# Kernel tuning notes

Hardware: AMD Instinct MI355X
Metric: run time of the kernel (lower is better)

Reference implementation:

```python
import jax, jax.numpy as jnp
import numpy as np

# ---- hyperparameters matching init_kwargs / input_specs ----
K = 16          # max neighbors kept per node (avg degree)
ALPHA = 0.5     # FGW trade-off (POT default used in the repo)
FW_ITERS = 5    # Frank-Wolfe (conditional-gradient) outer iterations
SK_ITERS = 20   # log-domain Sinkhorn inner iterations
REG = 0.1       # entropic regularization for the inner OT solve
NEG = -1e9      # "log(0)" for masked (padded) neighborhood slots


def build_neighbors(edge_index, n, k):
    """Fixed-size (padded) neighbor table from a COO edge list."""
    src, dst = edge_index[0], edge_index[1]
    order = jnp.argsort(src)
    s_src, s_dst = src[order], dst[order]
    ids = jnp.arange(n)
    start = jnp.searchsorted(s_src, ids)
    end = jnp.searchsorted(s_src, ids, side='right')
    cnt = jnp.minimum(end - start, k)                       # [n]
    pos = start[:, None] + jnp.arange(k)[None, :]           # [n,k]
    valid = jnp.arange(k)[None, :] < cnt[:, None]           # [n,k]
    nbrs = s_dst[jnp.clip(pos, 0, s_src.shape[0] - 1)]      # [n,k]
    return nbrs, valid


def reference(x, edge_index, templates, templates_features):
    n, d = x.shape
    nbrs, valid = build_neighbors(edge_index, n, K)
    # local node set per node: self + up to K neighbors -> K1 = K+1 slots
    S = jnp.concatenate([jnp.arange(n)[:, None], nbrs], axis=1)            # [n,K1]
    mask = jnp.concatenate([jnp.ones((n, 1), bool), valid], axis=1)        # [n,K1]
    mf = mask.astype(x.dtype)

    # local subgraph adjacency: A[i,a,b] = 1 iff edge S[i,a] -> S[i,b]
    nbrs_of = nbrs[S]                                                      # [n,K1,K]
    valid_of = valid[S]
    eq = (nbrs_of[:, :, None, :] == S[:, None, :, None]) & valid_of[:, :, None, :]
    C1 = eq.any(-1).astype(x.dtype) * mf[:, :, None] * mf[:, None, :]      # [n,K1,K1]

    F1 = x[S] * mf[:, :, None]                                             # [n,K1,d]
    F2 = templates_features                                                # [T,t,d]
    # squared-euclidean feature cost M[i,T,a,b] = ||F1[i,a]-F2[T,b]||^2
    M = (jnp.sum(F1 ** 2, -1)[:, None, :, None]
         + jnp.sum(F2 ** 2, -1)[None, :, None, :]
         - 2.0 * jnp.einsum('nad,tbd->ntab', F1, F2))                      # [n,T,K1,t]

    cnt1 = mf.sum(1)                                                       # [n] (>=1: self)
    p = mf / cnt1[:, None]                                                 # [n,K1] uniform masked
    t_n = templates.shape[1]
    q = jnp.full((t_n,), 1.0 / t_n, x.dtype)
    C2 = templates                                                         # [T,t,t]

    # GW square-loss decomposition (POT): tens = constC - 2*C1 @ T @ C2^T
    constC = (jnp.einsum('nab,nb->na', C1 ** 2, p)[:, None, :, None]
              + jnp.einsum('tab,b->ta', C2 ** 2, q)[None, :, None, :])     # [n,T,K1,t]

    def tens_of(T):
        tmp = jnp.einsum('nac,ntcd->ntad', C1, T)
        cross = jnp.einsum('ntad,tbd->ntab', tmp, C2)
        return constC - 2.0 * cross

    logp = jnp.where(mask, -jnp.log(cnt1)[:, None], NEG)[:, None, :]       # [n,1,K1]
    logq = -jnp.log(jnp.asarray(t_n, x.dtype))                             # scalar

    def sinkhorn(G):
        logK = -G / REG                                                    # [n,T,K1,t]
        f = jnp.zeros(G.shape[:3], G.dtype)
        g = jnp.zeros(G.shape[:2] + (t_n,), G.dtype)
        def body(_, fg):
            f, g = fg
            g = logq - jax.nn.logsumexp(logK + f[..., :, None], axis=-2)
            f = logp - jax.nn.logsumexp(logK + g[..., None, :], axis=-1)
            return (f, g)
        f, g = jax.lax.fori_loop(0, SK_ITERS, body, (f, g))
        return jnp.exp(f[..., :, None] + g[..., None, :] + logK)

    T0 = p[:, None, :, None] * q[None, None, None, :]                      # [n,1->T,K1,t]
    T0 = jnp.broadcast_to(T0, M.shape)

    def fw_step(T, k):
        tens = tens_of(T)
        G = (1.0 - ALPHA) * M + 2.0 * ALPHA * tens                         # FGW gradient
        Tn = sinkhorn(G)                                                   # linear-min oracle
        gamma = 2.0 / (k + 2.0)
        return (1.0 - gamma) * T + gamma * Tn, None

    T, _ = jax.lax.scan(fw_step, T0, jnp.arange(FW_ITERS, dtype=x.dtype))

    tens = tens_of(T)
    dist = ((1.0 - ALPHA) * jnp.sum(M * T, axis=(-2, -1))
            + ALPHA * jnp.sum(tens * T, axis=(-2, -1)))                    # [n,T]
    return dist


def setup_inputs() -> dict:
    key = jax.random.key(0)
    k1, k2, k3, k4 = jax.random.split(key, 4)
    n, d, e = 10000, 128, 160000
    n_T, t_n = 10, 10
    x = jax.random.normal(k1, (n, d), jnp.float32)
    edge_index = jax.random.randint(k2, (2, e), 0, n, jnp.int64)
    templates = jax.random.uniform(k3, (n_T, t_n, t_n), jnp.float32)
    templates_features = jax.random.normal(k4, (n_T, t_n, d), jnp.float32)
    return {"x": x, "edge_index": edge_index,
            "templates": templates, "templates_features": templates_features}
```

## Files before the change

### kernel.cpp

```cpp
#include <hip/hip_runtime.h>
#include <math.h>

#define NNODE 10000
#define NEDGE 160000
#define KNB   16
#define K1    17
#define NT    10
#define TN    10
#define DF    128
#define CAP   64
#define NEG_BIG (-1e9f)

#define LOGQ2      (-3.32192809489f)
#define KB_SCALE   (-14.4269504089f)
#define CR_SCALE   (28.8539008178f)
#define G_SCALE    (-0.069314718056f)
#define LN2        0.69314718056f
#define TINYF      1e-30f

#if defined(__has_builtin)
#if __has_builtin(__builtin_amdgcn_exp2f)
#define EXP2F(x) __builtin_amdgcn_exp2f(x)
#endif
#if __has_builtin(__builtin_amdgcn_rcpf)
#define RCPF(x) __builtin_amdgcn_rcpf(x)
#endif
#endif
#ifndef EXP2F
#define EXP2F(x) __expf((x) * LN2)
#endif
#ifndef RCPF
#define RCPF(x) (1.0f / (x))
#endif
#define LOG2F(x) __log2f(x)

#define WSYNC() asm volatile("s_waitcnt lgkmcnt(0)" ::: "memory")

__device__ __forceinline__ float2 pk_add(float2 a, float2 b) { return make_float2(a.x + b.x, a.y + b.y); }
__device__ __forceinline__ float2 pk_sub(float2 a, float2 b) { return make_float2(a.x - b.x, a.y - b.y); }
__device__ __forceinline__ float2 pk_mul(float2 a, float2 b) { return make_float2(a.x * b.x, a.y * b.y); }
__device__ __forceinline__ float2 pk_max(float2 a, float2 b) { return make_float2(fmaxf(a.x, b.x), fmaxf(a.y, b.y)); }
__device__ __forceinline__ float2 pk_fma(float2 a, float2 b, float2 c) { return make_float2(fmaf(a.x, b.x, c.x), fmaf(a.y, b.y, c.y)); }
__device__ __forceinline__ float2 pk_exp2(float2 a) { return make_float2(EXP2F(a.x), EXP2F(a.y)); }
__device__ __forceinline__ float clamp120(float x) { return fminf(120.f, fmaxf(-120.f, x)); }

__device__ __forceinline__ int detect_wide(const int* ei) {
  int z = 0;
#pragma unroll
  for (int i = 0; i < 32; ++i) z |= ei[2 * i + 1];
  return z == 0;
}

__global__ void __launch_bounds__(256) k_prep(const int* __restrict__ ei,
                                              int* cnt, int* ebuf,
                                              const float* __restrict__ x,
                                              const float* __restrict__ tf,
                                              const float* __restrict__ tmpl,
                                              float* __restrict__ dots,
                                              float* __restrict__ nxv,
                                              float* __restrict__ nF2,
                                              float* __restrict__ Bq) {
  __shared__ float xs[64][DF];
  const int tid = threadIdx.x;
  if (blockIdx.x < 625) {
    int e = blockIdx.x * 256 + tid;
    int wide = detect_wide(ei);
    int s = wide ? ei[2 * e] : ei[e];
    int pos = atomicAdd(&cnt[s], 1);
    if (pos < CAP) ebuf[s * CAP + pos] = e;
    return;
  }
  const int db = blockIdx.x - 625;
  if (db == 0 && tid < NT * TN) {
    const float* fp = tf + (size_t)tid * DF;
    float s = 0.f;
    for (int d = 0; d < DF; ++d) { float v = fp[d]; s += v * v; }
    nF2[tid] = s;
    const float* cp = tmpl + (size_t)tid * TN;
    float s2 = 0.f;
    for (int c = 0; c < TN; ++c) { float v = cp[c]; s2 += v * v; }
    Bq[tid] = 0.1f * s2;
  }
  const int nb = db * 64;
  const int nvalid = (NNODE - nb) < 64 ? (NNODE - nb) : 64;
  {
    const float4* xg = (const float4*)(x + (size_t)nb * DF);
    float4* xl = (float4*)&xs[0][0];
    for (int i = tid; i < nvalid * (DF / 4); i += 256) xl[i] = xg[i];
  }
  __syncthreads();
  for (int o = tid; o < nvalid * (NT * TN); o += 256) {
    int n = o / (NT * TN);
    int tb = o - n * (NT * TN);
    const float4* fp = (const float4*)(tf + (size_t)tb * DF);
    const float4* xp = (const float4*)&xs[n][0];
    float s = 0.f;
#pragma unroll
    for (int d = 0; d < DF / 4; ++d) {
      float4 a = xp[d], f = fp[d];
      s += a.x * f.x + a.y * f.y + a.z * f.z + a.w * f.w;
    }
    dots[(size_t)(nb + n) * (NT * TN) + tb] = s;
  }
  if (tid < nvalid) {
    const float4* xp = (const float4*)&xs[tid][0];
    float s = 0.f;
#pragma unroll
    for (int d = 0; d < DF / 4; ++d) {
      float4 a = xp[d];
      s += a.x * a.x + a.y * a.y + a.z * a.z + a.w * a.w;
    }
    nxv[nb + tid] = s;
  }
}

__global__ void k_select(const int* ei, const int* cnt, const int* ebuf,
                         int* nbrs, int* kcnt, int* Sg) {
  int i = blockIdx.x * blockDim.x + threadIdx.x;
  if (i >= NNODE) return;
  int wide = detect_wide(ei);
  int c = cnt[i]; c = c > CAP ? CAP : c;
  int best[KNB];
  int m = 0;
  for (int j = 0; j < c; ++j) {
    int e = ebuf[i * CAP + j];
    if (m < KNB) {
      int p = m++;
      while (p > 0 && best[p - 1] > e) { best[p] = best[p - 1]; --p; }
      best[p] = e;
    } else if (e < best[KNB - 1]) {
      int p = KNB - 1;
      while (p > 0 && best[p - 1] > e) { best[p] = best[p - 1]; --p; }
      best[p] = e;
    }
  }
  kcnt[i] = m;
  Sg[i * K1 + 0] = i;
  for (int j = 0; j < KNB; ++j) {
    int v = 0;
    if (j < m) {
      int e = best[j];
      v = wide ? ei[2 * (NEDGE + e)] : ei[NEDGE + e];
    }
    nbrs[i * KNB + j] = v;
    Sg[i * K1 + 1 + j] = v;
  }
}

__global__ void __launch_bounds__(256) k_c1b(const int* __restrict__ nbrs,
                                             const int* __restrict__ kcnt,
                                             const int* __restrict__ Sg,
                                             unsigned int* __restrict__ bitsG,
                                             float* __restrict__ Ag) {
  int idx = blockIdx.x * 256 + threadIdx.x;
  if (idx >= NNODE * K1) return;
  int i = idx / K1;
  int a = idx - i * K1;
  int kc = kcnt[i];
  unsigned int vmask = (kc >= KNB) ? 0x1FFFFu : ((2u << kc) - 1u);
  unsigned int bits = 0;
  bool va = (a == 0) || (a - 1 < kc);
  if (va) {
    int S[K1];
#pragma unroll
    for (int b = 0; b < K1; ++b) S[b] = Sg[i * K1 + b];
    int u = S[a];
    int ku = kcnt[u];
    const int* np = nbrs + (size_t)u * KNB;
    for (int j = 0; j < ku; ++j) {
      int w = np[j];
#pragma unroll
      for (int b = 0; b < K1; ++b) bits |= (S[b] == w) ? (1u << b) : 0u;
    }
    bits &= vmask;
  }
  bitsG[idx] = bits;
  Ag[idx] = (float)__popc(bits) / (float)(1 + kc);
}

__global__ void __launch_bounds__(128, 3) k_main(
    const float* __restrict__ tmpl,
    const int* __restrict__ kcnt, const int* __restrict__ Sg,
    const unsigned int* __restrict__ bitsG, const float* __restrict__ Ag,
    const float* __restrict__ dots, const float* __restrict__ nxv,
    const float* __restrict__ nF2, const float* __restrict__ Bq,
    float* __restrict__ out)
{
  __shared__ float KT[2 * 5 * 244];
  __shared__ float fL[2][5][20];
  __shared__ float gL[2][5][12];
  __shared__ float accL[2][5][TN];
  __shared__ float uL[2][5][20];
  __shared__ float wL[2][5][12];

  const int wv = threadIdx.x >> 6;
  const int lane = threadIdx.x & 63;
  int p = lane / 10;
  const int b = lane - p * 10;
  const bool act = (p < 5);
  if (!act) p = 4;
  const int node = blockIdx.x;
  const int t = wv * 5 + p;
  const int tb = t * TN + b;
  float* KTp = &KT[(wv * 5 + p) * 244];

  const int kc = kcnt[node];
  const float cnt1 = (float)(1 + kc);
  const float inv_cnt1 = 1.f / cnt1;
  const float logp2v = -LOG2F(cnt1);
  const float lp2_r0 = ((b == 0) || (b - 1 < kc)) ? logp2v : NEG_BIG;
  const float lp2_r1 = ((9 + b) < kc) ? logp2v : NEG_BIG;

  float2 c2v[5];
  {
    const float2* cp = (const float2*)(tmpl + (size_t)tb * TN);
#pragma unroll
    for (int j = 0; j < 5; ++j) c2v[j] = cp[j];
  }
  const float Bb = Bq[tb];
  const float nf2b = nF2[tb];

  float2 Kb2v[8]; float kb16;
  float2 Tpv[8];  float tp16;
  unsigned int bw[K1];
#pragma unroll
  for (int a = 0; a < K1; ++a) {
    bool va = (a == 0) || (a - 1 < kc);
    int sa = Sg[node * K1 + a];
    float Ma = (va ? (nxv[sa] - 2.f * dots[(size_t)sa * (NT * TN) + tb]) : 0.f) + nf2b;
    float base = 0.5f * Ma + Ag[node * K1 + a] + Bb;
    float kv = KB_SCALE * base;
    float tv = va ? (inv_cnt1 * 0.1f) : 0.f;
    if (a == 16) { kb16 = kv; tp16 = tv; }
    else if (a & 1) { Kb2v[a >> 1].y = kv; Tpv[a >> 1].y = tv; }
    else { Kb2v[a >> 1].x = kv; Tpv[a >> 1].x = tv; }
    bw[a] = bitsG[node * K1 + a];
  }

  float2 Kc2v[8]; float k16 = 0.f;
  float2 Kr0v[5], Kr1v[5];
  float2 gr[5];
  float g2 = 0.f, fr0 = 0.f, fr1 = 0.f;

#pragma unroll 1
  for (int k = 0; k < 6; ++k) {
    if (act) {
#pragma unroll
      for (int a = 0; a < 16; ++a) KTp[a * 12 + b] = (a & 1) ? Tpv[a >> 1].y : Tpv[a >> 1].x;
      KTp[16 * 12 + b] = tp16;
    }
    WSYNC();
    float R[K1];
#pragma unroll
    for (int c = 0; c < K1; ++c) {
      const float* row = &KTp[c * 12];
      float4 u0 = *(const float4*)row;
      float4 u1 = *(const float4*)(row + 4);
      float2 u2 = *(const float2*)(row + 8);
      float2 acc = pk_mul(make_float2(u0.x, u0.y), c2v[0]);
      acc = pk_fma(make_float2(u0.z, u0.w), c2v[1], acc);
      acc = pk_fma(make_float2(u1.x, u1.y), c2v[2], acc);
      acc = pk_fma(make_float2(u1.z, u1.w), c2v[3], acc);
      acc = pk_fma(u2, c2v[4], acc);
      R[c] = acc.x + acc.y;
    }
#pragma unroll
    for (int a = 0; a < K1; ++a) {
      float cr = 0.f;
      unsigned int m = bw[a];
      if (m) {
#pragma unroll
        for (int c = 0; c < K1; ++c)
          if (m & (1u << c)) cr += R[c];
      }
      float base = (a == 16) ? kb16 : ((a & 1) ? Kb2v[a >> 1].y : Kb2v[a >> 1].x);
      float val = base + CR_SCALE * cr;
      if (a == 16) k16 = val;
      else if (a & 1) Kc2v[a >> 1].y = val;
      else Kc2v[a >> 1].x = val;
    }

    if (k == 5) {
      float acc = 0.f;
#pragma unroll
      for (int a = 0; a < K1; ++a) {
        bool va = (a == 0) || (a - 1 < kc);
        int sa = Sg[node * K1 + a];
        float Ma = (va ? (nxv[sa] - 2.f * dots[(size_t)sa * (NT * TN) + tb]) : 0.f) + nf2b;
        float kcv = (a == 16) ? k16 : ((a & 1) ? Kc2v[a >> 1].y : Kc2v[a >> 1].x);
        float tpv = (a == 16) ? tp16 : ((a & 1) ? Tpv[a >> 1].y : Tpv[a >> 1].x);
        acc += tpv * (0.25f * Ma + 0.5f * (G_SCALE * kcv));
      }
      if (act) accL[wv][p][b] = acc;
      WSYNC();
      if (lane < 5) {
        float s = 0.f;
#pragma unroll
        for (int j = 0; j < TN; ++j) s += accL[wv][lane][j];
        out[node * NT + wv * 5 + lane] = s;
      }
      return;
    }

    WSYNC();
    if (act) {
#pragma unroll
      for (int a = 0; a < 16; ++a) KTp[a * 12 + b] = (a & 1) ? Kc2v[a >> 1].y : Kc2v[a >> 1].x;
      KTp[16 * 12 + b] = k16;
    }
    WSYNC();
    {
      const float* r0 = &KTp[b * 12];
      float4 u0 = *(const float4*)r0;
      float4 u1 = *(const float4*)(r0 + 4);
      float2 u2 = *(const float2*)(r0 + 8);
      Kr0v[0] = make_float2(u0.x, u0.y); Kr0v[1] = make_float2(u0.z, u0.w);
      Kr0v[2] = make_float2(u1.x, u1.y); Kr0v[3] = make_float2(u1.z, u1.w);
      Kr0v[4] = u2;
      const float* r1 = &KTp[(10 + b) * 12];
      float4 w0 = *(const float4*)r1;
      float4 w1 = *(const float4*)(r1 + 4);
      float2 w2 = *(const float2*)(r1 + 8);
      Kr1v[0] = make_float2(w0.x, w0.y); Kr1v[1] = make_float2(w0.z, w0.w);
      Kr1v[2] = make_float2(w1.x, w1.y); Kr1v[3] = make_float2(w1.z, w1.w);
      Kr1v[4] = w2;
    }

#pragma unroll 1
    for (int it = 0; it < 2; ++it) {
      float2 v[8]; float v16;
      if (it == 0) {
#pragma unroll
        for (int i = 0; i < 8; ++i) v[i] = Kc2v[i];
        v16 = k16;
      } else {
        float4 f0 = *(const float4*)&fL[wv][p][0];
        float4 f1 = *(const float4*)&fL[wv][p][4];
        float4 f2 = *(const float4*)&fL[wv][p][8];
        float4 f3 = *(const float4*)&fL[wv][p][12];
        float fx = fL[wv][p][16];
        v[0] = pk_add(Kc2v[0], make_float2(f0.x, f0.y));
        v[1] = pk_add(Kc2v[1], make_float2(f0.z, f0.w));
        v[2] = pk_add(Kc2v[2], make_float2(f1.x, f1.y));
        v[3] = pk_add(Kc2v[3], make_float2(f1.z, f1.w));
        v[4] = pk_add(Kc2v[4], make_float2(f2.x, f2.y));
        v[5] = pk_add(Kc2v[5], make_float2(f2.z, f2.w));
        v[6] = pk_add(Kc2v[6], make_float2(f3.x, f3.y));
        v[7] = pk_add(Kc2v[7], make_float2(f3.z, f3.w));
        v16 = k16 + fx;
      }
      float2 m01 = pk_max(pk_max(v[0], v[1]), pk_max(v[2], v[3]));
      float2 m23 = pk_max(pk_max(v[4], v[5]), pk_max(v[6], v[7]));
      float2 mm = pk_max(m01, m23);
      float mx = fmaxf(fmaxf(mm.x, mm.y), v16);
      float2 mxb = make_float2(mx, mx);
      float2 ss = pk_exp2(pk_sub(v[0], mxb));
      ss = pk_add(ss, pk_exp2(pk_sub(v[1], mxb)));
      ss = pk_add(ss, pk_exp2(pk_sub(v[2], mxb)));
      ss = pk_add(ss, pk_exp2(pk_sub(v[3], mxb)));
      ss = pk_add(ss, pk_exp2(pk_sub(v[4], mxb)));
      ss = pk_add(ss, pk_exp2(pk_sub(v[5], mxb)));
      ss = pk_add(ss, pk_exp2(pk_sub(v[6], mxb)));
      ss = pk_add(ss, pk_exp2(pk_sub(v[7], mxb)));
      float s = ss.x + ss.y + EXP2F(v16 - mx);
      g2 = LOGQ2 - mx - LOG2F(s);
      if (act) gL[wv][p][b] = g2;
      WSYNC();
      {
        float4 g0 = *(const float4*)&gL[wv][p][0];
        float4 g1 = *(const float4*)&gL[wv][p][4];
        float2 gx = *(const float2*)&gL[wv][p][8];
        gr[0] = make_float2(g0.x, g0.y); gr[1] = make_float2(g0.z, g0.w);
        gr[2] = make_float2(g1.x, g1.y); gr[3] = make_float2(g1.z, g1.w);
        gr[4] = gx;
      }
      float2 w0[5], w1[5];
#pragma unroll
      for (int j = 0; j < 5; ++j) w0[j] = pk_add(Kr0v[j], gr[j]);
#pragma unroll
      for (int j = 0; j < 5; ++j) w1[j] = pk_add(Kr1v[j], gr[j]);
      float2 a01 = pk_max(pk_max(w0[0], w0[1]), pk_max(w0[2], w0[3]));
      a01 = pk_max(a01, w0[4]);
      float mxa = fmaxf(a01.x, a01.y);
      float2 b01 = pk_max(pk_max(w1[0], w1[1]), pk_max(w1[2], w1[3]));
      b01 = pk_max(b01, w1[4]);
      float mxb2 = fmaxf(b01.x, b01.y);
      float2 mab = make_float2(mxa, mxa);
      float2 mbb = make_float2(mxb2, mxb2);
      float2 sx = pk_exp2(pk_sub(w0[0], mab));
      sx = pk_add(sx, pk_exp2(pk_sub(w0[1], mab)));
      sx = pk_add(sx, pk_exp2(pk_sub(w0[2], mab)));
      sx = pk_add(sx, pk_exp2(pk_sub(w0[3], mab)));
      sx = pk_add(sx, pk_exp2(pk_sub(w0[4], mab)));
      float2 sy = pk_exp2(pk_sub(w1[0], mbb));
      sy = pk_add(sy, pk_exp2(pk_sub(w1[1], mbb)));
      sy = pk_add(sy, pk_exp2(pk_sub(w1[2], mbb)));
      sy = pk_add(sy, pk_exp2(pk_sub(w1[3], mbb)));
      sy = pk_add(sy, pk_exp2(pk_sub(w1[4], mbb)));
      fr0 = lp2_r0 - mxa - LOG2F(sx.x + sx.y);
      fr1 = lp2_r1 - mxb2 - LOG2F(sy.x + sy.y);
      if (act) {
        fL[wv][p][b] = fr0;
        if (b < 7) fL[wv][p][10 + b] = fr1;
      }
      WSYNC();
    }

    float2 Kcsv[8]; float kcs16;
    float P00, P01, Q0;
    float2 Krs01[10];
    {
      float4 F0 = *(const float4*)&fL[wv][p][0];
      float4 F1 = *(const float4*)&fL[wv][p][4];
      float4 F2 = *(const float4*)&fL[wv][p][8];
      float4 F3 = *(const float4*)&fL[wv][p][12];
      float f16v = fL[wv][p][16];
      float2 q[8];
      q[0] = pk_add(Kc2v[0], make_float2(F0.x, F0.y));
      q[1] = pk_add(Kc2v[1], make_float2(F0.z, F0.w));
      q[2] = pk_add(Kc2v[2], make_float2(F1.x, F1.y));
      q[3] = pk_add(Kc2v[3], make_float2(F1.z, F1.w));
      q[4] = pk_add(Kc2v[4], make_float2(F2.x, F2.y));
      q[5] = pk_add(Kc2v[5], make_float2(F2.z, F2.w));
      q[6] = pk_add(Kc2v[6], make_float2(F3.x, F3.y));
      q[7] = pk_add(Kc2v[7], make_float2(F3.z, F3.w));
      float q16 = k16 + f16v;
      float2 qm = pk_max(pk_max(pk_max(q[0], q[1]), pk_max(q[2], q[3])),
                         pk_max(pk_max(q[4], q[5]), pk_max(q[6], q[7])));
      float sigma = fmaxf(fmaxf(qm.x, qm.y), q16);
      float2 sgb = make_float2(sigma, sigma);
#pragma unroll
      for (int i = 0; i < 8; ++i) Kcsv[i] = pk_exp2(pk_sub(q[i], sgb));
      kcs16 = EXP2F(q16 - sigma);
      Q0 = EXP2F(clamp120(LOGQ2 - sigma - g2));
      float2 a0[5], a1[5];
#pragma unroll
      for (int j = 0; j < 5; ++j) a0[j] = pk_add(Kr0v[j], gr[j]);
#pragma unroll
      for (int j = 0; j < 5; ++j) a1[j] = pk_add(Kr1v[j], gr[j]);
      float2 r0m = pk_max(pk_max(a0[0], a0[1]), pk_max(a0[2], a0[3]));
      r0m = pk_max(r0m, a0[4]);
      float rho0 = fmaxf(r0m.x, r0m.y);
      float2 r1m = pk_max(pk_max(a1[0], a1[1]), pk_max(a1[2], a1[3]));
      r1m = pk_max(r1m, a1[4]);
      float rho1 = fmaxf(r1m.x, r1m.y);
#pragma unroll
      for (int j = 0; j < 5; ++j) {
        Krs01[2 * j]     = make_float2(EXP2F(a0[j].x - rho0), EXP2F(a1[j].x - rho1));
        Krs01[2 * j + 1] = make_float2(EXP2F(a0[j].y - rho0), EXP2F(a1[j].y - rho1));
      }
      P00 = EXP2F(clamp120((lp2_r0 - rho0) - fr0));
      P01 = EXP2F(clamp120((lp2_r1 - rho1) - fr1));
    }

    float Slast, t0, t1;
    {
      float2 S2 = pk_add(pk_add(pk_add(Kcsv[0], Kcsv[1]), pk_add(Kcsv[2], Kcsv[3])),
                         pk_add(pk_add(Kcsv[4], Kcsv[5]), pk_add(Kcsv[6], Kcsv[7])));
      float S = fmaxf(S2.x + S2.y + kcs16, TINYF);
      Slast = S;
      float wb = Q0 * RCPF(S);
      if (act) wL[wv][p][b] = wb;
      WSYNC();
      float4 W0 = *(const float4*)&wL[wv][p][0];
      float4 W1 = *(const float4*)&wL[wv][p][4];
      float2 W2 = *(const float2*)&wL[wv][p][8];
      float2 t01 = pk_mul(Krs01[0], make_float2(W0.x, W0.x));
      t01 = pk_fma(Krs01[1], make_float2(W0.y, W0.y), t01);
      t01 = pk_fma(Krs01[2], make_float2(W0.z, W0.z), t01);
      t01 = pk_fma(Krs01[3], make_float2(W0.w, W0.w), t01);
      t01 = pk_fma(Krs01[4], make_float2(W1.x, W1.x), t01);
      t01 = pk_fma(Krs01[5], make_float2(W1.y, W1.y), t01);
      t01 = pk_fma(Krs01[6], make_float2(W1.z, W1.z), t01);
      t01 = pk_fma(Krs01[7], make_float2(W1.w, W1.w), t01);
      t01 = pk_fma(Krs01[8], make_float2(W2.x, W2.x), t01);
      t01 = pk_fma(Krs01[9], make_float2(W2.y, W2.y), t01);
      t0 = t01.x; t1 = t01.y;
    }
#pragma unroll 1
    for (int it = 0; it < 17; ++it) {
      float u0 = P00 * RCPF(fmaxf(t0, TINYF));
      float u1 = P01 * RCPF(fmaxf(t1, TINYF));
      if (act) {
        uL[wv][p][b] = u0;
        if (b < 7) uL[wv][p][10 + b] = u1;
      }
      WSYNC();
      float4 U0 = *(const float4*)&uL[wv][p][0];
      float4 U1 = *(const float4*)&uL[wv][p][4];
      float4 U2 = *(const float4*)&uL[wv][p][8];
      float4 U3 = *(const float4*)&uL[wv][p][12];
      float u16f = uL[wv][p][16];
      float2 S2 = pk_mul(Kcsv[0], make_float2(U0.x, U0.y));
      S2 = pk_fma(Kcsv[1], make_float2(U0.z, U0.w), S2);
      S2 = pk_fma(Kcsv[2], make_float2(U1.x, U1.y), S2);
      S2 = pk_fma(Kcsv[3], make_float2(U1.z, U1.w), S2);
      S2 = pk_fma(Kcsv[4], make_float2(U2.x, U2.y), S2);
      S2 = pk_fma(Kcsv[5], make_float2(U2.z, U2.w), S2);
      S2 = pk_fma(Kcsv[6], make_float2(U3.x, U3.y), S2);
      S2 = pk_fma(Kcsv[7], make_float2(U3.z, U3.w), S2);
      float S = fmaxf(S2.x + S2.y + kcs16 * u16f, TINYF);
      Slast = S;
      float wb = Q0 * RCPF(S);
      if (act) wL[wv][p][b] = wb;
      WSYNC();
      float4 W0 = *(const float4*)&wL[wv][p][0];
      float4 W1 = *(const float4*)&wL[wv][p][4];
      float2 W2 = *(const float2*)&wL[wv][p][8];
      float2 t01 = pk_mul(Krs01[0], make_float2(W0.x, W0.x));
      t01 = pk_fma(Krs01[1], make_float2(W0.y, W0.y), t01);
      t01 = pk_fma(Krs01[2], make_float2(W0.z, W0.z), t01);
      t01 = pk_fma(Krs01[3], make_float2(W0.w, W0.w), t01);
      t01 = pk_fma(Krs01[4], make_float2(W1.x, W1.x), t01);
      t01 = pk_fma(Krs01[5], make_float2(W1.y, W1.y), t01);
      t01 = pk_fma(Krs01[6], make_float2(W1.z, W1.z), t01);
      t01 = pk_fma(Krs01[7], make_float2(W1.w, W1.w), t01);
      t01 = pk_fma(Krs01[8], make_float2(W2.x, W2.x), t01);
      t01 = pk_fma(Krs01[9], make_float2(W2.y, W2.y), t01);
      t0 = t01.x; t1 = t01.y;
    }

    {
      float u0 = P00 * RCPF(fmaxf(t0, TINYF));
      float u1 = P01 * RCPF(fmaxf(t1, TINYF));
      if (act) {
        uL[wv][p][b] = u0;
        if (b < 7) uL[wv][p][10 + b] = u1;
      }
      WSYNC();
      float4 U0 = *(const float4*)&uL[wv][p][0];
      float4 U1 = *(const float4*)&uL[wv][p][4];
      float4 U2 = *(const float4*)&uL[wv][p][8];
      float4 U3 = *(const float4*)&uL[wv][p][12];
      float u16f = uL[wv][p][16];
      const float sb = 0.1f * RCPF(Slast);
      const float gam = 2.f / ((float)k + 2.f);
      const float om = 1.f - gam;
      const float gs = gam * sb;
      const float2 omb = make_float2(om, om);
      const float2 gsb = make_float2(gs, gs);
      float2 uu[8];
      uu[0] = make_float2(U0.x, U0.y); uu[1] = make_float2(U0.z, U0.w);
      uu[2] = make_float2(U1.x, U1.y); uu[3] = make_float2(U1.z, U1.w);
      uu[4] = make_float2(U2.x, U2.y); uu[5] = make_float2(U2.z, U2.w);
      uu[6] = make_float2(U3.x, U3.y); uu[7] = make_float2(U3.z, U3.w);
#pragma unroll
      for (int i = 0; i < 8; ++i)
        Tpv[i] = pk_fma(omb, Tpv[i], pk_mul(gsb, pk_mul(Kcsv[i], uu[i])));
      tp16 = om * tp16 + gs * kcs16 * u16f;
    }
  }
}

extern "C" void kernel_launch(void* const* d_in, const int* in_sizes, int n_in,
                              void* d_out, int out_size, void* d_ws, size_t ws_size,
                              hipStream_t stream) {
  const float* x    = (const float*)d_in[0];
  const int*   ei   = (const int*)d_in[1];
  const float* tmpl = (const float*)d_in[2];
  const float* tf   = (const float*)d_in[3];
  float* out = (float*)d_out;

  int* cnt  = (int*)d_ws;
  int* ebuf = cnt + NNODE;
  int* nbrs = ebuf + (size_t)NNODE * CAP;
  int* kcnt = nbrs + (size_t)NNODE * KNB;
  int* Sg   = kcnt + NNODE;
  unsigned int* bits = (unsigned int*)(Sg + (size_t)NNODE * K1);
  float* Ag   = (float*)(bits + (size_t)NNODE * K1);
  float* dots = Ag + (size_t)NNODE * K1;
  float* nxv  = dots + (size_t)NNODE * (NT * TN);
  float* nF2  = nxv + NNODE;
  float* Bq   = nF2 + NT * TN;

  hipMemsetAsync(cnt, 0, NNODE * sizeof(int), stream);
  k_prep<<<625 + (NNODE + 63) / 64, 256, 0, stream>>>(ei, cnt, ebuf, x, tf, tmpl,
                                                      dots, nxv, nF2, Bq);
  k_select<<<(NNODE + 255) / 256, 256, 0, stream>>>(ei, cnt, ebuf, nbrs, kcnt, Sg);
  k_c1b<<<(NNODE * K1 + 255) / 256, 256, 0, stream>>>(nbrs, kcnt, Sg, bits, Ag);
  k_main<<<NNODE, 128, 0, stream>>>(tmpl, kcnt, Sg, bits, Ag, dots, nxv, nF2, Bq, out);
}
```

Before: 605.6 us.

## Pack two nodes per 256-thread block and interleave u/T vectors as pairs

k_main now handles two nodes per block with 256 threads, and launch bounds change to (256,5) to raise occupancy. Per-wave LDS strides shrink from 244 to 204 floats. The transport plan and scaled-kernel registers are repacked into a 10-entry float2 layout pairing row j with row j+10. This lets u values be written as one float2 store and read as five float4 loads instead of scalar stores with a tail element. The tighter register budget implied by the new launch bound risks spills in a register-heavy kernel.

```diff
diff --git a/kernel.cpp b/kernel.cpp
--- a/kernel.cpp
+++ b/kernel.cpp
@@ -178,7 +178,7 @@
   Ag[idx] = (float)__popc(bits) / (float)(1 + kc);
 }
 
-__global__ void __launch_bounds__(128, 3) k_main(
+__global__ void __launch_bounds__(256, 5) k_main(
     const float* __restrict__ tmpl,
     const int* __restrict__ kcnt, const int* __restrict__ Sg,
     const unsigned int* __restrict__ bitsG, const float* __restrict__ Ag,
@@ -186,12 +186,12 @@
     const float* __restrict__ nF2, const float* __restrict__ Bq,
     float* __restrict__ out)
 {
-  __shared__ float KT[2 * 5 * 244];
-  __shared__ float fL[2][5][20];
-  __shared__ float gL[2][5][12];
-  __shared__ float accL[2][5][TN];
-  __shared__ float uL[2][5][20];
-  __shared__ float wL[2][5][12];
+  __shared__ float KT[4 * 5 * 204 + 48];
+  __shared__ float fL[4][5][20];
+  __shared__ float gL[4][5][12];
+  __shared__ float uL[4][5][20];
+  __shared__ float wL[4][5][12];
+  __shared__ float accL[4][5][TN];
 
   const int wv = threadIdx.x >> 6;
   const int lane = threadIdx.x & 63;
@@ -199,10 +199,11 @@
   const int b = lane - p * 10;
   const bool act = (p < 5);
   if (!act) p = 4;
-  const int node = blockIdx.x;
-  const int t = wv * 5 + p;
+  const int node = blockIdx.x * 2 + (wv >> 1);
+  const int h = wv & 1;
+  const int t = h * 5 + p;
   const int tb = t * TN + b;
-  float* KTp = &KT[(wv * 5 + p) * 244];
+  float* KTp = &KT[(wv * 5 + p) * 204];
 
   const int kc = kcnt[node];
   const float cnt1 = (float)(1 + kc);
@@ -221,7 +222,9 @@
   const float nf2b = nF2[tb];
 
   float2 Kb2v[8]; float kb16;
-  float2 Tpv[8];  float tp16;
+  float2 Tp2[10];
+#pragma unroll
+  for (int j = 0; j < 10; ++j) Tp2[j] = make_float2(0.f, 0.f);
   unsigned int bw[K1];
 #pragma unroll
   for (int a = 0; a < K1; ++a) {
@@ -231,9 +234,10 @@
     float base = 0.5f * Ma + Ag[node * K1 + a] + Bb;
     float kv = KB_SCALE * base;
     float tv = va ? (inv_cnt1 * 0.1f) : 0.f;
-    if (a == 16) { kb16 = kv; tp16 = tv; }
-    else if (a & 1) { Kb2v[a >> 1].y = kv; Tpv[a >> 1].y = tv; }
-    else { Kb2v[a >> 1].x = kv; Tpv[a >> 1].x = tv; }
+    if (a == 16) kb16 = kv;
+    else if (a & 1) Kb2v[a >> 1].y = kv;
+    else Kb2v[a >> 1].x = kv;
+    if (a < 10) Tp2[a].x = tv; else Tp2[a - 10].y = tv;
     bw[a] = bitsG[node * K1 + a];
   }
 
@@ -246,8 +250,8 @@
   for (int k = 0; k < 6; ++k) {
     if (act) {
 #pragma unroll
-      for (int a = 0; a < 16; ++a) KTp[a * 12 + b] = (a & 1) ? Tpv[a >> 1].y : Tpv[a >> 1].x;
-      KTp[16 * 12 + b] = tp16;
+      for (int a = 0; a < K1; ++a)
+        KTp[a * 12 + b] = (a < 10) ? Tp2[a].x : Tp2[a - 10].y;
     }
     WSYNC();
     float R[K1];
@@ -288,7 +292,7 @@
         int sa = Sg[node * K1 + a];
         float Ma = (va ? (nxv[sa] - 2.f * dots[(size_t)sa * (NT * TN) + tb]) : 0.f) + nf2b;
         float kcv = (a == 16) ? k16 : ((a & 1) ? Kc2v[a >> 1].y : Kc2v[a >> 1].x);
-        float tpv = (a == 16) ? tp16 : ((a & 1) ? Tpv[a >> 1].y : Tpv[a >> 1].x);
+        float tpv = (a < 10) ? Tp2[a].x : Tp2[a - 10].y;
         acc += tpv * (0.25f * Ma + 0.5f * (G_SCALE * kcv));
       }
       if (act) accL[wv][p][b] = acc;
@@ -297,7 +301,7 @@
         float s = 0.f;
 #pragma unroll
         for (int j = 0; j < TN; ++j) s += accL[wv][lane][j];
-        out[node * NT + wv * 5 + lane] = s;
+        out[node * NT + h * 5 + lane] = s;
       }
       return;
     }
@@ -406,7 +410,7 @@
       WSYNC();
     }
 
-    float2 Kcsv[8]; float kcs16;
+    float2 Kcs2[10];
     float P00, P01, Q0;
     float2 Krs01[10];
     {
@@ -415,23 +419,27 @@
       float4 F2 = *(const float4*)&fL[wv][p][8];
       float4 F3 = *(const float4*)&fL[wv][p][12];
       float f16v = fL[wv][p][16];
-      float2 q[8];
-      q[0] = pk_add(Kc2v[0], make_float2(F0.x, F0.y));
-      q[1] = pk_add(Kc2v[1], make_float2(F0.z, F0.w));
-      q[2] = pk_add(Kc2v[2], make_float2(F1.x, F1.y));
-      q[3] = pk_add(Kc2v[3], make_float2(F1.z, F1.w));
-      q[4] = pk_add(Kc2v[4], make_float2(F2.x, F2.y));
-      q[5] = pk_add(Kc2v[5], make_float2(F2.z, F2.w));
-      q[6] = pk_add(Kc2v[6], make_float2(F3.x, F3.y));
-      q[7] = pk_add(Kc2v[7], make_float2(F3.z, F3.w));
-      float q16 = k16 + f16v;
-      float2 qm = pk_max(pk_max(pk_max(q[0], q[1]), pk_max(q[2], q[3])),
-                         pk_max(pk_max(q[4], q[5]), pk_max(q[6], q[7])));
-      float sigma = fmaxf(fmaxf(qm.x, qm.y), q16);
-      float2 sgb = make_float2(sigma, sigma);
-#pragma unroll
-      for (int i = 0; i < 8; ++i) Kcsv[i] = pk_exp2(pk_sub(q[i], sgb));
-      kcs16 = EXP2F(q16 - sigma);
+      float fs[K1];
+      fs[0] = F0.x; fs[1] = F0.y; fs[2] = F0.z; fs[3] = F0.w;
+      fs[4] = F1.x; fs[5] = F1.y; fs[6] = F1.z; fs[7] = F1.w;
+      fs[8] = F2.x; fs[9] = F2.y; fs[10] = F2.z; fs[11] = F2.w;
+      fs[12] = F3.x; fs[13] = F3.y; fs[14] = F3.z; fs[15] = F3.w;
+      fs[16] = f16v;
+      float qs[K1];
+#pragma unroll
+      for (int a = 0; a < K1; ++a) {
+        float kcv = (a == 16) ? k16 : ((a & 1) ? Kc2v[a >> 1].y : Kc2v[a >> 1].x);
+        qs[a] = kcv + fs[a];
+      }
+      float sigma = qs[0];
+#pragma unroll
+      for (int a = 1; a < K1; ++a) sigma = fmaxf(sigma, qs[a]);
+#pragma unroll
+      for (int j = 0; j < 10; ++j) {
+        float kx = EXP2F(qs[j] - sigma);
+        float ky = (j < 7) ? EXP2F(qs[10 + j] - sigma) : 0.f;
+        Kcs2[j] = make_float2(kx, ky);
+      }
       Q0 = EXP2F(clamp120(LOGQ2 - sigma - g2));
       float2 a0[5], a1[5];
 #pragma unroll
@@ -455,9 +463,10 @@
 
     float Slast, t0, t1;
     {
-      float2 S2 = pk_add(pk_add(pk_add(Kcsv[0], Kcsv[1]), pk_add(Kcsv[2], Kcsv[3])),
-                         pk_add(pk_add(Kcsv[4], Kcsv[5]), pk_add(Kcsv[6], Kcsv[7])));
-      float S = fmaxf(S2.x + S2.y + kcs16, TINYF);
+      float2 S2 = pk_add(pk_add(pk_add(Kcs2[0], Kcs2[1]), pk_add(Kcs2[2], Kcs2[3])),
+                         pk_add(pk_add(Kcs2[4], Kcs2[5]), pk_add(Kcs2[6], Kcs2[7])));
+      S2 = pk_add(S2, pk_add(Kcs2[8], Kcs2[9]));
+      float S = fmaxf(S2.x + S2.y, TINYF);
       Slast = S;
       float wb = Q0 * RCPF(S);
       if (act) wL[wv][p][b] = wb;
@@ -481,25 +490,24 @@
     for (int it = 0; it < 17; ++it) {
       float u0 = P00 * RCPF(fmaxf(t0, TINYF));
       float u1 = P01 * RCPF(fmaxf(t1, TINYF));
-      if (act) {
-        uL[wv][p][b] = u0;
-        if (b < 7) uL[wv][p][10 + b] = u1;
-      }
+      if (act) *(float2*)&uL[wv][p][2 * b] = make_float2(u0, u1);
       WSYNC();
       float4 U0 = *(const float4*)&uL[wv][p][0];
       float4 U1 = *(const float4*)&uL[wv][p][4];
       float4 U2 = *(const float4*)&uL[wv][p][8];
       float4 U3 = *(const float4*)&uL[wv][p][12];
-      float u16f = uL[wv][p][16];
-      float2 S2 = pk_mul(Kcsv[0], make_float2(U0.x, U0.y));
-      S2 = pk_fma(Kcsv[1], make_float2(U0.z, U0.w), S2);
-      S2 = pk_fma(Kcsv[2], make_float2(U1.x, U1.y), S2);
-      S2 = pk_fma(Kcsv[3], make_float2(U1.z, U1.w), S2);
-      S2 = pk_fma(Kcsv[4], make_float2(U2.x, U2.y), S2);
-      S2 = pk_fma(Kcsv[5], make_float2(U2.z, U2.w), S2);
-      S2 = pk_fma(Kcsv[6], make_float2(U3.x, U3.y), S2);
-      S2 = pk_fma(Kcsv[7], make_float2(U3.z, U3.w), S2);
-      float S = fmaxf(S2.x + S2.y + kcs16 * u16f, TINYF);
+      float4 U4 = *(const float4*)&uL[wv][p][16];
+      float2 S2 = pk_mul(Kcs2[0], make_float2(U0.x, U0.y));
+      S2 = pk_fma(Kcs2[1], make_float2(U0.z, U0.w), S2);
+      S2 = pk_fma(Kcs2[2], make_float2(U1.x, U1.y), S2);
+      S2 = pk_fma(Kcs2[3], make_float2(U1.z, U1.w), S2);
+      S2 = pk_fma(Kcs2[4], make_float2(U2.x, U2.y), S2);
+      S2 = pk_fma(Kcs2[5], make_float2(U2.z, U2.w), S2);
+      S2 = pk_fma(Kcs2[6], make_float2(U3.x, U3.y), S2);
+      S2 = pk_fma(Kcs2[7], make_float2(U3.z, U3.w), S2);
+      S2 = pk_fma(Kcs2[8], make_float2(U4.x, U4.y), S2);
+      S2 = pk_fma(Kcs2[9], make_float2(U4.z, U4.w), S2);
+      float S = fmaxf(S2.x + S2.y, TINYF);
       Slast = S;
       float wb = Q0 * RCPF(S);
       if (act) wL[wv][p][b] = wb;
@@ -523,31 +531,27 @@
     {
       float u0 = P00 * RCPF(fmaxf(t0, TINYF));
       float u1 = P01 * RCPF(fmaxf(t1, TINYF));
-      if (act) {
-        uL[wv][p][b] = u0;
-        if (b < 7) uL[wv][p][10 + b] = u1;
-      }
+      if (act) *(float2*)&uL[wv][p][2 * b] = make_float2(u0, u1);
       WSYNC();
       float4 U0 = *(const float4*)&uL[wv][p][0];
       float4 U1 = *(const float4*)&uL[wv][p][4];
       float4 U2 = *(const float4*)&uL[wv][p][8];
       float4 U3 = *(const float4*)&uL[wv][p][12];
-      float u16f = uL[wv][p][16];
-      const float sb = 0.1f * RCPF(Slast);
+      float4 U4 = *(const float4*)&uL[wv][p][16];
       const float gam = 2.f / ((float)k + 2.f);
+      const float gs = gam * 0.1f * RCPF(Slast);
       const float om = 1.f - gam;
-      const float gs = gam * sb;
       const float2 omb = make_float2(om, om);
       const float2 gsb = make_float2(gs, gs);
-      float2 uu[8];
+      float2 uu[10];
       uu[0] = make_float2(U0.x, U0.y); uu[1] = make_float2(U0.z, U0.w);
       uu[2] = make_float2(U1.x, U1.y); uu[3] = make_float2(U1.z, U1.w);
       uu[4] = make_float2(U2.x, U2.y); uu[5] = make_float2(U2.z, U2.w);
       uu[6] = make_float2(U3.x, U3.y); uu[7] = make_float2(U3.z, U3.w);
-#pragma unroll
-      for (int i = 0; i < 8; ++i)
-        Tpv[i] = pk_fma(omb, Tpv[i], pk_mul(gsb, pk_mul(Kcsv[i], uu[i])));
-      tp16 = om * tp16 + gs * kcs16 * u16f;
+      uu[8] = make_float2(U4.x, U4.y); uu[9] = make_float2(U4.z, U4.w);
+#pragma unroll
+      for (int j = 0; j < 10; ++j)
+        Tp2[j] = pk_fma(omb, Tp2[j], pk_mul(gsb, pk_mul(Kcs2[j], uu[j])));
     }
   }
 }
@@ -578,5 +582,5 @@
                                                       dots, nxv, nF2, Bq);
   k_select<<<(NNODE + 255) / 256, 256, 0, stream>>>(ei, cnt, ebuf, nbrs, kcnt, Sg);
   k_c1b<<<(NNODE * K1 + 255) / 256, 256, 0, stream>>>(nbrs, kcnt, Sg, bits, Ag);
-  k_main<<<NNODE, 128, 0, stream>>>(tmpl, kcnt, Sg, bits, Ag, dots, nxv, nF2, Bq, out);
+  k_main<<<NNODE / 2, 256, 0, stream>>>(tmpl, kcnt, Sg, bits, Ag, dots, nxv, nF2, Bq, out);
 }
```

Result: slower. 1.083 ms (+78.8%).
